# Kernel tuning notes

Measured on AMD Instinct MI355X. Metric: run time of the kernel, lower is better.

Reference implementation:

```python
import jax, jax.numpy as jnp
import numpy as np

N = 65536   # number of GP locations
M = 64      # max ancestor set size (contiguous window A(i) = {i-M+1..i})
B = 16384   # minibatch size


def setup_inputs() -> dict:
    rng = np.random.default_rng(0)
    i = np.arange(N)
    # CSR row lengths: U (lower-tri) row i has cols {max(0,i-M+1)..i}; V (upper-tri) row j has cols {j..min(j+M-1,N-1)}
    row_len_u = np.minimum(i + 1, M)
    row_len_v = np.minimum(M, N - i)
    crow_u = np.concatenate([[0], np.cumsum(row_len_u)]).astype(np.int32)
    crow_v = np.concatenate([[0], np.cumsum(row_len_v)]).astype(np.int32)
    nnz = int(crow_u[-1])  # 4192288, same for both matrices
    # off-diagonals small, diagonals near 1 (kept positive for logDet and solve stability)
    U_values = (rng.standard_normal(nnz) * 0.1).astype(np.float32)
    U_values[crow_u[1:] - 1] = rng.uniform(0.8, 1.2, N).astype(np.float32)  # last entry of row i = (i,i)
    V_values = (rng.standard_normal(nnz) * 0.1).astype(np.float32)
    V_values[crow_v[:-1]] = rng.uniform(0.8, 1.2, N).astype(np.float32)    # first entry of row i = (i,i)
    mean = (rng.standard_normal(N) * 0.5).astype(np.float32)
    mean_post = (rng.standard_normal(N) * 0.5).astype(np.float32)
    y = rng.standard_normal(N).astype(np.float32)
    mini_indices = rng.integers(0, N, B).astype(np.int32)
    return {
        'U_values': jnp.asarray(U_values),
        'V_values': jnp.asarray(V_values),
        'mean': jnp.asarray(mean),
        'mean_post': jnp.asarray(mean_post),
        'y': jnp.asarray(y),
        'noise': jnp.float32(0.1),
        'mini_indices': jnp.asarray(mini_indices),
        'crow_u': jnp.asarray(crow_u),
        'crow_v': jnp.asarray(crow_v),
    }


def reference(U_values, V_values, mean, mean_post, y, noise, mini_indices, crow_u, crow_v):
    nnz = U_values.shape[0]
    g = mini_indices                       # [B] selected rows
    L = jnp.minimum(g + 1, M)              # n_anc per selected row
    p = jnp.arange(M)
    valid = p[None, :] >= (M - L)[:, None]                 # [B,M] right-aligned validity mask
    anc = g[:, None] - (M - 1 - p)[None, :]                # global ancestor index at padded slot p
    anc_c = jnp.clip(anc, 0, N - 1)

    # get_sub_rows(UTrans): row g entries at A(g), right-aligned into [B,M]
    u_idx = crow_u[g][:, None] + (p[None, :] - (M - L)[:, None])
    U_sub = jnp.where(valid, U_values[jnp.clip(u_idx, 0, nnz - 1)], 0.0)

    # ragged mean difference gather (masked scatter in the original)
    md = jnp.where(valid, (mean - mean_post)[anc_c], 0.0)  # [B,M]

    # get_sub_mat(V, unit_diag=True): V[A(g),A(g)] bottom-right aligned, identity padding
    jrow = anc_c[:, :, None]                               # global row index of block row r
    icol = anc_c[:, None, :]                               # global col index of block col c
    vidx = crow_v[jrow] + (icol - jrow)                    # CSR value index of V[jrow, icol]
    blk_mask = (valid[:, :, None] & valid[:, None, :]
                & (p[None, :, None] <= p[None, None, :]))  # upper-tri of active block
    eye = jnp.eye(M, dtype=U_values.dtype)
    V_sub = jnp.where(blk_mask, V_values[jnp.clip(vidx, 0, nnz - 1)], eye[None, :, :])  # [B,M,M]

    # batched triangular solves
    ej = jnp.zeros((B, M), U_values.dtype).at[:, -1].set(1.0)
    sol_e = jax.scipy.linalg.solve_triangular(V_sub, ej[:, :, None], lower=False)
    marginalVarPost = jnp.sum(sol_e * sol_e, axis=(1, 2))  # [B]
    sol_u = jax.scipy.linalg.solve_triangular(V_sub, U_sub[:, :, None], lower=False)
    innerCov = -0.5 * jnp.sum(sol_u * sol_u)

    innerMean = -0.5 * jnp.sum(jnp.sum(U_sub * md, axis=1) ** 2)

    # log-determinant terms from diagonal gathers
    logDet = (jnp.sum(jnp.log(U_values[crow_u[g + 1] - 1]))
              - jnp.sum(jnp.log(V_values[crow_v[g]])))

    # Gaussian expected likelihood (noise is not None branch)
    resid = y[g] - mean_post[g]
    ell = (-0.5 * B * jnp.log(2.0 * jnp.pi * noise)
           - (jnp.sum(resid * resid) + jnp.sum(marginalVarPost)) / (2.0 * noise))

    return logDet + innerMean + innerCov + ell
```

## Files before the change

### kernel.cpp

```cpp
#include <hip/hip_runtime.h>
#include <math.h>

constexpr int kN = 65536;
constexpr int kB = 16384;
constexpr int kTileW = 2560;

static __device__ __forceinline__ float bcastf(float v, int lane) {
    union { float f; int i; } u;
    u.f = v;
    u.i = __builtin_amdgcn_readlane(u.i, lane);
    return u.f;
}

static __device__ __forceinline__ void gload_lds16(const float* g, float* l) {
    __builtin_amdgcn_global_load_lds(
        (const __attribute__((address_space(1))) void*)g,
        (__attribute__((address_space(3))) void*)l, 16, 0, 0);
}
static __device__ __forceinline__ void gload_lds4(const float* g, float* l) {
    __builtin_amdgcn_global_load_lds(
        (const __attribute__((address_space(1))) void*)g,
        (__attribute__((address_space(3))) void*)l, 4, 0, 0);
}

static __device__ __forceinline__ int row_start(int j) {
    const int t = j >> 4;
    return 1024 * t - 128 * t * (t - 1) + (64 - 16 * t) * (j - 16 * t);
}

__global__ __launch_bounds__(64) void gp_solve_kernel(
    const float* __restrict__ Uv,
    const float* __restrict__ Vv,
    const float* __restrict__ mean,
    const float* __restrict__ mean_post,
    const float* __restrict__ y,
    const int*   __restrict__ gidx,
    const int*   __restrict__ crow_u,
    const int*   __restrict__ crow_v,
    const float* __restrict__ noise,
    float*       __restrict__ partial)
{
    __shared__ __align__(16) float myl[kTileW];

    const int lane = (int)threadIdx.x;
    const int b    = (int)blockIdx.x;
    const int g    = gidx[b];

    const int  anc = g - 63 + lane;
    const bool vl  = (anc >= 0);
    const bool hot = (g >= 63) && (g <= kN - 63);

    const int L  = (g + 1 < 64) ? (g + 1) : 64;
    const int ub = (g >= 63) ? (2016 + 64 * (g - 63)) : crow_u[g];

    float uval = 0.0f, md = 0.0f;
    if (vl) {
        uval = Uv[ub + lane - (64 - L)];
        md   = mean[anc] - mean_post[anc];
    }
    const float yg  = y[g];
    const float mpg = mean_post[g];

    if (hot) {
        const float* base = Vv + 64 * (g - 63);
        {
            const float* src = base + 4 * lane;
            #pragma unroll
            for (int k = 0; k < 4; ++k)
                gload_lds16(src + 256 * k, myl + 256 * k);
        }
        #pragma unroll
        for (int k = 0; k < 3; ++k) {
            const int w   = 256 * k + 4 * lane;
            const int jj  = ((w >> 4) * 171) >> 9;
            const int col = w - 48 * jj;
            gload_lds16(base + 64 * (16 + jj) + col, myl + 1024 + 256 * k);
        }
        #pragma unroll
        for (int k = 0; k < 2; ++k) {
            const int w = 256 * k + 4 * lane;
            gload_lds16(base + 64 * (32 + (w >> 5)) + (w & 31), myl + 1792 + 256 * k);
        }
        {
            const int w = 4 * lane;
            gload_lds16(base + 64 * (48 + (w >> 4)) + (w & 15), myl + 2304);
        }
    } else {
        int rowbase = 0;
        if (vl) rowbase = crow_v[anc];
        for (int j = 0; j < 64; ++j) {
            union { float f; int i; } rb; rb.i = __builtin_amdgcn_readlane(rowbase, j);
            const int dst = row_start(j);
            if (lane < 64 - j) {
                if (g - 63 + j >= 0)
                    gload_lds4(Vv + rb.i + lane, myl + dst);
                else
                    myl[dst + lane] = 0.0f;
            }
        }
    }
    asm volatile("s_waitcnt vmcnt(0) lgkmcnt(0)" ::: "memory");

    const int rs = row_start(lane);
    const float d0   = myl[rs];
    const float diag = vl ? d0 : 1.0f;
    const float invd = 1.0f / diag;

    const float* vrow = myl + (rs - lane);
    float v[64];
    #pragma unroll
    for (int i = 0; i < 64; ++i) v[i] = vrow[i];

    float r_e = (lane == 63) ? 1.0f : 0.0f;
    float r_u = uval;
    float acc_e = 0.0f, acc_u = 0.0f;

    #pragma unroll
    for (int i = 63; i >= 0; --i) {
        const float t_e = r_e * invd;
        const float t_u = r_u * invd;
        const float s_e = bcastf(t_e, i);
        const float s_u = bcastf(t_u, i);
        r_e = fmaf(-v[i], s_e, r_e);
        r_u = fmaf(-v[i], s_u, r_u);
        acc_e = fmaf(s_e, s_e, acc_e);
        acc_u = fmaf(s_u, s_u, acc_u);
    }

    float dot = uval * md;
    #pragma unroll
    for (int m = 1; m < 64; m <<= 1)
        dot += __shfl_xor(dot, m, 64);

    const float ulast  = bcastf(uval, 63);
    const float vfirst = bcastf(diag, 63);

    if (lane == 0) {
        const float resid = yg - mpg;
        const float inv2n = 0.5f / noise[0];
        partial[b] = logf(ulast) - logf(vfirst)
                   - 0.5f * dot * dot
                   - 0.5f * acc_u
                   - (resid * resid + acc_e) * inv2n;
    }
}

__global__ __launch_bounds__(1024) void gp_reduce_kernel(
    const float* __restrict__ partial,
    const float* __restrict__ noise,
    float*       __restrict__ out)
{
    __shared__ float ws[16];
    const int t = (int)threadIdx.x;
    float a = 0.0f;
    #pragma unroll
    for (int k = 0; k < 4; ++k) {
        const float4 p = reinterpret_cast<const float4*>(partial)[t + 1024 * k];
        a += (p.x + p.y) + (p.z + p.w);
    }
    #pragma unroll
    for (int m = 1; m < 64; m <<= 1)
        a += __shfl_xor(a, m, 64);
    if ((t & 63) == 0) ws[t >> 6] = a;
    __syncthreads();
    if (t == 0) {
        float tot = 0.0f;
        #pragma unroll
        for (int k = 0; k < 16; ++k) tot += ws[k];
        tot += -0.5f * (float)kB * logf(2.0f * 3.14159265358979323846f * noise[0]);
        out[0] = tot;
    }
}

extern "C" void kernel_launch(void* const* d_in, const int* in_sizes, int n_in,
                              void* d_out, int out_size, void* d_ws, size_t ws_size,
                              hipStream_t stream)
{
    const float* Uv        = (const float*)d_in[0];
    const float* Vv        = (const float*)d_in[1];
    const float* mean      = (const float*)d_in[2];
    const float* mean_post = (const float*)d_in[3];
    const float* y         = (const float*)d_in[4];
    const float* noise     = (const float*)d_in[5];
    const int*   gidx      = (const int*)d_in[6];
    const int*   crow_u    = (const int*)d_in[7];
    const int*   crow_v    = (const int*)d_in[8];
    float* partial = (float*)d_ws;

    gp_solve_kernel<<<dim3(kB), dim3(64), 0, stream>>>(
        Uv, Vv, mean, mean_post, y, gidx, crow_u, crow_v, noise, partial);
    gp_reduce_kernel<<<dim3(1), dim3(1024), 0, stream>>>(
        partial, noise, (float*)d_out);
}
```

Baseline: 38.63 us.

## Process two samples per wavefront, overlapping second tile load with first solve

Each 64-thread block now handles two minibatch rows, with two LDS tiles. Both tiles' V loads are issued up front, and a partial vmcnt wait lets the first triangular solve start while the second tile is still in flight. This hides global-load latency and halves the block count and partial-sum count. It also prescales V rows by the inverse diagonal to drop two multiplies per step and swaps logf for __logf. In exchange it doubles LDS per block (which may cut occupancy), and the vmcnt(10) count is tied to the exact number of loads issued, so it is fragile.

```diff
diff --git a/kernel.cpp b/kernel.cpp
--- a/kernel.cpp
+++ b/kernel.cpp
@@ -4,6 +4,7 @@
 constexpr int kN = 65536;
 constexpr int kB = 16384;
 constexpr int kTileW = 2560;
+constexpr int kElems = 2;
 
 static __device__ __forceinline__ float bcastf(float v, int lane) {
     union { float f; int i; } u;
@@ -26,6 +27,119 @@
 static __device__ __forceinline__ int row_start(int j) {
     const int t = j >> 4;
     return 1024 * t - 128 * t * (t - 1) + (64 - 16 * t) * (j - 16 * t);
+}
+
+static __device__ __forceinline__ bool is_hot(int g) {
+    return (g >= 63) && (g <= kN - 63);
+}
+
+struct EState { float uval, md, yg, mpg; };
+
+static __device__ __forceinline__ EState stage_one(
+    int g, int lane, float* myl,
+    const float* __restrict__ Uv, const float* __restrict__ Vv,
+    const float* __restrict__ mean, const float* __restrict__ mean_post,
+    const float* __restrict__ y, const int* __restrict__ crow_u,
+    const int* __restrict__ crow_v)
+{
+    const int  anc = g - 63 + lane;
+    const bool vl  = (anc >= 0);
+    const int  L   = (g + 1 < 64) ? (g + 1) : 64;
+    const int  ub  = (g >= 63) ? (2016 + 64 * (g - 63)) : crow_u[g];
+
+    EState s;
+    s.uval = 0.0f; s.md = 0.0f;
+    if (vl) {
+        s.uval = Uv[ub + lane - (64 - L)];
+        s.md   = mean[anc] - mean_post[anc];
+    }
+    s.yg  = y[g];
+    s.mpg = mean_post[g];
+
+    if (is_hot(g)) {
+        const float* base = Vv + 64 * (g - 63);
+        {
+            const float* src = base + 4 * lane;
+            #pragma unroll
+            for (int k = 0; k < 4; ++k)
+                gload_lds16(src + 256 * k, myl + 256 * k);
+        }
+        #pragma unroll
+        for (int k = 0; k < 3; ++k) {
+            const int w   = 256 * k + 4 * lane;
+            const int jj  = ((w >> 4) * 171) >> 9;
+            const int col = w - 48 * jj;
+            gload_lds16(base + 64 * (16 + jj) + col, myl + 1024 + 256 * k);
+        }
+        #pragma unroll
+        for (int k = 0; k < 2; ++k) {
+            const int w = 256 * k + 4 * lane;
+            gload_lds16(base + 64 * (32 + (w >> 5)) + (w & 31), myl + 1792 + 256 * k);
+        }
+        {
+            const int w = 4 * lane;
+            gload_lds16(base + 64 * (48 + (w >> 4)) + (w & 15), myl + 2304);
+        }
+    } else {
+        int rowbase = 0;
+        if (vl) rowbase = crow_v[anc];
+        for (int j = 0; j < 64; ++j) {
+            const int rbj = __builtin_amdgcn_readlane(rowbase, j);
+            const int dst = row_start(j);
+            if (lane < 64 - j) {
+                if (g - 63 + j >= 0)
+                    gload_lds4(Vv + rbj + lane, myl + dst);
+                else
+                    myl[dst + lane] = 0.0f;
+            }
+        }
+    }
+    return s;
+}
+
+static __device__ __forceinline__ float compute_one(
+    int g, int lane, const float* myl, EState st, float inv2n)
+{
+    const int  anc = g - 63 + lane;
+    const bool vl  = (anc >= 0);
+
+    const int rs = row_start(lane);
+    const float d0   = myl[rs];
+    const float diag = vl ? d0 : 1.0f;
+    const float invd = 1.0f / diag;
+
+    const float* vrow = myl + (rs - lane);
+    float v[64];
+    #pragma unroll
+    for (int i = 0; i < 64; ++i) v[i] = vrow[i] * invd;
+
+    float r_e = (lane == 63) ? invd : 0.0f;
+    float r_u = st.uval * invd;
+    float acc_e = 0.0f, acc_u = 0.0f;
+
+    #pragma unroll
+    for (int i = 63; i >= 0; --i) {
+        const float s_e = bcastf(r_e, i);
+        const float s_u = bcastf(r_u, i);
+        r_e = fmaf(-v[i], s_e, r_e);
+        r_u = fmaf(-v[i], s_u, r_u);
+        acc_e = fmaf(s_e, s_e, acc_e);
+        acc_u = fmaf(s_u, s_u, acc_u);
+    }
+
+    float dot = st.uval * st.md;
+    #pragma unroll
+    for (int m = 1; m < 64; m <<= 1)
+        dot += __shfl_xor(dot, m, 64);
+
+    const float ulast  = bcastf(st.uval, 63);
+    const float vfirst = bcastf(diag, 63);
+
+    const float resid = st.yg - st.mpg;
+    return __logf(ulast) - __logf(vfirst)
+         - 0.5f * dot * dot
+         - 0.5f * acc_u
+         - (resid * resid + acc_e) * inv2n;
 }
 
 __global__ __launch_bounds__(64) void gp_solve_kernel(
@@ -40,109 +154,30 @@
     const float* __restrict__ noise,
     float*       __restrict__ partial)
 {
-    __shared__ __align__(16) float myl[kTileW];
+    __shared__ __align__(16) float lds[kElems][kTileW];
 
     const int lane = (int)threadIdx.x;
-    const int b    = (int)blockIdx.x;
-    const int g    = gidx[b];
-
-    const int  anc = g - 63 + lane;
-    const bool vl  = (anc >= 0);
-    const bool hot = (g >= 63) && (g <= kN - 63);
-
-    const int L  = (g + 1 < 64) ? (g + 1) : 64;
-    const int ub = (g >= 63) ? (2016 + 64 * (g - 63)) : crow_u[g];
-
-    float uval = 0.0f, md = 0.0f;
-    if (vl) {
-        uval = Uv[ub + lane - (64 - L)];
-        md   = mean[anc] - mean_post[anc];
-    }
-    const float yg  = y[g];
-    const float mpg = mean_post[g];
-
-    if (hot) {
-        const float* base = Vv + 64 * (g - 63);
-        {
-            const float* src = base + 4 * lane;
-            #pragma unroll
-            for (int k = 0; k < 4; ++k)
-                gload_lds16(src + 256 * k, myl + 256 * k);
-        }
-        #pragma unroll
-        for (int k = 0; k < 3; ++k) {
-            const int w   = 256 * k + 4 * lane;
-            const int jj  = ((w >> 4) * 171) >> 9;
-            const int col = w - 48 * jj;
-            gload_lds16(base + 64 * (16 + jj) + col, myl + 1024 + 256 * k);
-        }
-        #pragma unroll
-        for (int k = 0; k < 2; ++k) {
-            const int w = 256 * k + 4 * lane;
-            gload_lds16(base + 64 * (32 + (w >> 5)) + (w & 31), myl + 1792 + 256 * k);
-        }
-        {
-            const int w = 4 * lane;
-            gload_lds16(base + 64 * (48 + (w >> 4)) + (w & 15), myl + 2304);
-        }
-    } else {
-        int rowbase = 0;
-        if (vl) rowbase = crow_v[anc];
-        for (int j = 0; j < 64; ++j) {
-            union { float f; int i; } rb; rb.i = __builtin_amdgcn_readlane(rowbase, j);
-            const int dst = row_start(j);
-            if (lane < 64 - j) {
-                if (g - 63 + j >= 0)
-                    gload_lds4(Vv + rb.i + lane, myl + dst);
-                else
-                    myl[dst + lane] = 0.0f;
-            }
-        }
-    }
+    const int b0   = (int)blockIdx.x * kElems;
+    const int g0   = gidx[b0];
+    const int g1   = gidx[b0 + 1];
+
+    EState s0 = stage_one(g0, lane, lds[0], Uv, Vv, mean, mean_post, y, crow_u, crow_v);
+    asm volatile("" ::: "memory");
+    EState s1 = stage_one(g1, lane, lds[1], Uv, Vv, mean, mean_post, y, crow_u, crow_v);
+
+    const float inv2n = 0.5f / noise[0];
+
+    if (is_hot(g0) && is_hot(g1))
+        asm volatile("s_waitcnt vmcnt(10) lgkmcnt(0)" ::: "memory");
+    else
+        asm volatile("s_waitcnt vmcnt(0) lgkmcnt(0)" ::: "memory");
+    const float c0 = compute_one(g0, lane, lds[0], s0, inv2n);
+
     asm volatile("s_waitcnt vmcnt(0) lgkmcnt(0)" ::: "memory");
-
-    const int rs = row_start(lane);
-    const float d0   = myl[rs];
-    const float diag = vl ? d0 : 1.0f;
-    const float invd = 1.0f / diag;
-
-    const float* vrow = myl + (rs - lane);
-    float v[64];
-    #pragma unroll
-    for (int i = 0; i < 64; ++i) v[i] = vrow[i];
-
-    float r_e = (lane == 63) ? 1.0f : 0.0f;
-    float r_u = uval;
-    float acc_e = 0.0f, acc_u = 0.0f;
-
-    #pragma unroll
-    for (int i = 63; i >= 0; --i) {
-        const float t_e = r_e * invd;
-        const float t_u = r_u * invd;
-        const float s_e = bcastf(t_e, i);
-        const float s_u = bcastf(t_u, i);
-        r_e = fmaf(-v[i], s_e, r_e);
-        r_u = fmaf(-v[i], s_u, r_u);
-        acc_e = fmaf(s_e, s_e, acc_e);
-        acc_u = fmaf(s_u, s_u, acc_u);
-    }
-
-    float dot = uval * md;
-    #pragma unroll
-    for (int m = 1; m < 64; m <<= 1)
-        dot += __shfl_xor(dot, m, 64);
-
-    const float ulast  = bcastf(uval, 63);
-    const float vfirst = bcastf(diag, 63);
-
-    if (lane == 0) {
-        const float resid = yg - mpg;
-        const float inv2n = 0.5f / noise[0];
-        partial[b] = logf(ulast) - logf(vfirst)
-                   - 0.5f * dot * dot
-                   - 0.5f * acc_u
-                   - (resid * resid + acc_e) * inv2n;
-    }
+    const float c1 = compute_one(g1, lane, lds[1], s1, inv2n);
+
+    if (lane == 0)
+        partial[blockIdx.x] = c0 + c1;
 }
 
 __global__ __launch_bounds__(1024) void gp_reduce_kernel(
@@ -154,7 +189,7 @@
     const int t = (int)threadIdx.x;
     float a = 0.0f;
     #pragma unroll
-    for (int k = 0; k < 4; ++k) {
+    for (int k = 0; k < 2; ++k) {
         const float4 p = reinterpret_cast<const float4*>(partial)[t + 1024 * k];
         a += (p.x + p.y) + (p.z + p.w);
     }
@@ -187,7 +222,7 @@
     const int*   crow_v    = (const int*)d_in[8];
     float* partial = (float*)d_ws;
 
-    gp_solve_kernel<<<dim3(kB), dim3(64), 0, stream>>>(
+    gp_solve_kernel<<<dim3(kB / kElems), dim3(64), 0, stream>>>(
         Uv, Vv, mean, mean_post, y, gidx, crow_u, crow_v, noise, partial);
     gp_reduce_kernel<<<dim3(1), dim3(1024), 0, stream>>>(
         partial, noise, (float*)d_out);
```

New measurement: 49.14 us. 27.2% more time.
